# Kernel optimization log

Measured on AMD Instinct MI355X. Metric: run time of the kernel, lower is better.

## Reference

```python
import jax, jax.numpy as jnp
import numpy as np

N_NODES = 50000
N_EDGES = 800000
D_IN = 128
D_OUT = 128


def setup_inputs() -> dict:
    key = jax.random.key(0)
    k1, k2, k3, k4 = jax.random.split(key, 4)
    feature = jax.random.normal(k1, (N_NODES, D_IN), dtype=jnp.float32)
    edge_src = jax.random.randint(k2, (N_EDGES,), 0, N_NODES, dtype=jnp.int32)
    edge_dst = jax.random.randint(k3, (N_EDGES,), 0, N_NODES, dtype=jnp.int32)
    W = jax.random.normal(k4, (D_IN, D_OUT), dtype=jnp.float32) * (1.0 / np.sqrt(D_IN))
    b = jnp.zeros((D_OUT,), dtype=jnp.float32)
    return {"feature": feature, "edge_src": edge_src, "edge_dst": edge_dst, "W": W, "b": b}


def reference(feature, edge_src, edge_dst, W, b):
    # copy_src + sum reduce: for each edge, copy src node feature, sum into dst node
    msgs = feature[edge_src]  # [E, D_IN] gather
    h = jax.ops.segment_sum(msgs, edge_dst, num_segments=N_NODES)  # [N, D_IN]
    # linear + activation (relu)
    return jax.nn.relu(h @ W + b)
```

## Files before the change

kernel.cpp:

```cpp
#include <hip/hip_runtime.h>
#include <hip/hip_fp16.h>


constexpr int N    = 50000;
constexpr int E    = 800000;
constexpr int D    = 128;
constexpr int CAP  = 64;
constexpr int NT   = 3125;
constexpr int ZSTR = 136;
constexpr int NR   = 196;
constexpr int HB   = 256;
constexpr int EPB  = E / HB;

using f16x8 = __attribute__((ext_vector_type(8))) _Float16;
using f32x4 = __attribute__((ext_vector_type(4))) float;

__global__ void setup(const float* __restrict__ W, _Float16* __restrict__ Wf) {
    int t = blockIdx.x * 256 + threadIdx.x;
    int ct = t >> 8, ks = (t >> 6) & 3, lane = t & 63;
    int q = lane >> 4, li = lane & 15;
    _Float16 v[8];
    #pragma unroll
    for (int j = 0; j < 8; ++j)
        v[j] = (_Float16)W[(ks * 32 + q * 8 + j) * D + ct * 16 + li];
    *(f16x8*)(Wf + (size_t)t * 8) = *(const f16x8*)v;
}

__global__ __launch_bounds__(256) void midk(
        const float* __restrict__ feature,
        const int*   __restrict__ edst,
        const _Float16* __restrict__ Wf,
        int* __restrict__ hist,
        _Float16* __restrict__ Z) {
    __shared__ int h[NR];
    __shared__ _Float16 zs[4][16 * ZSTR];
    const int tid = threadIdx.x;

    if (blockIdx.x < HB) {
        const int b = blockIdx.x;
        if (tid < NR) h[tid] = 0;
        __syncthreads();
        const int e0 = b * EPB;
        for (int i = tid; i < EPB; i += 256)
            atomicAdd(&h[edst[e0 + i] >> 8], 1);
        __syncthreads();
        if (tid < NR) hist[b * NR + tid] = h[tid];
        return;
    }

    const int wave = tid >> 6, lane = tid & 63;
    const int wt = (blockIdx.x - HB) * 4 + wave;
    if (wt >= NT) return;
    const int q = lane >> 4, li = lane & 15;

    const float* fp = feature + (size_t)(wt * 16 + li) * D + q * 8;
    f16x8 afr[4];
    #pragma unroll
    for (int ks = 0; ks < 4; ++ks) {
        const float4 u0 = *(const float4*)(fp + ks * 32);
        const float4 u1 = *(const float4*)(fp + ks * 32 + 4);
        afr[ks][0] = (_Float16)u0.x; afr[ks][1] = (_Float16)u0.y;
        afr[ks][2] = (_Float16)u0.z; afr[ks][3] = (_Float16)u0.w;
        afr[ks][4] = (_Float16)u1.x; afr[ks][5] = (_Float16)u1.y;
        afr[ks][6] = (_Float16)u1.z; afr[ks][7] = (_Float16)u1.w;
    }

    f32x4 acc[8];
    #pragma unroll
    for (int ct = 0; ct < 8; ++ct) acc[ct] = (f32x4){0.f, 0.f, 0.f, 0.f};
    #pragma unroll
    for (int ks = 0; ks < 4; ++ks)
        #pragma unroll
        for (int ct = 0; ct < 8; ++ct) {
            const f16x8 b = *(const f16x8*)(Wf + (size_t)((ct * 4 + ks) * 64 + lane) * 8);
            acc[ct] = __builtin_amdgcn_mfma_f32_16x16x32_f16(afr[ks], b, acc[ct], 0, 0, 0);
        }

    _Float16* zt = zs[wave];
    #pragma unroll
    for (int ct = 0; ct < 8; ++ct)
        #pragma unroll
        for (int r = 0; r < 4; ++r)
            zt[(q * 4 + r) * ZSTR + ct * 16 + li] = (_Float16)acc[ct][r];
    #pragma unroll
    for (int it = 0; it < 4; ++it) {
        const f16x8 v = *(const f16x8*)(zt + (it * 4 + q) * ZSTR + li * 8);
        *(f16x8*)(Z + (size_t)(wt * 16 + it * 4 + q) * D + li * 8) = v;
    }
}

__global__ void scank(int* __restrict__ hist, int* __restrict__ total) {
    const int r    = blockIdx.x;
    const int lane = threadIdx.x;
    int h[4], sum = 0;
    #pragma unroll
    for (int j = 0; j < 4; ++j) {
        h[j] = hist[(lane * 4 + j) * NR + r];
        sum += h[j];
    }
    int incl = sum;
    #pragma unroll
    for (int off = 1; off < 64; off <<= 1) {
        int u = __shfl_up(incl, off);
        if (lane >= off) incl += u;
    }
    int run = incl - sum;
    #pragma unroll
    for (int j = 0; j < 4; ++j) {
        hist[(lane * 4 + j) * NR + r] = run;
        run += h[j];
    }
    if (lane == 63) total[r] = run;
}

__global__ __launch_bounds__(256) void partk(
        const int* __restrict__ esrc,
        const int* __restrict__ edst,
        const int* __restrict__ blockBase,
        const int* __restrict__ total,
        int* __restrict__ rangeStartG,
        unsigned int* __restrict__ part) {
    __shared__ int rs[NR];
    __shared__ int mb[NR];
    __shared__ int rk[NR];
    const int tid = threadIdx.x;
    const int b   = blockIdx.x;

    if (tid < 64) {
        int carry = 0;
        #pragma unroll
        for (int c = 0; c < 4; ++c) {
            int idx = c * 64 + tid;
            int v = (idx < NR) ? total[idx] : 0;
            int incl = v;
            #pragma unroll
            for (int off = 1; off < 64; off <<= 1) {
                int u = __shfl_up(incl, off);
                if (tid >= off) incl += u;
            }
            if (idx < NR) rs[idx] = incl - v + carry;
            carry += __shfl(incl, 63);
        }
    }
    if (tid < NR) { mb[tid] = blockBase[b * NR + tid]; rk[tid] = 0; }
    __syncthreads();
    if (b == 0 && tid < NR) rangeStartG[tid] = rs[tid];

    const int e0 = b * EPB;
    for (int i = tid; i < EPB; i += 256) {
        const int s = esrc[e0 + i];
        const int d = edst[e0 + i];
        const int r = d >> 8;
        const int k = atomicAdd(&rk[r], 1);
        part[rs[r] + mb[r] + k] = ((unsigned)(d & 255) << 16) | (unsigned)s;
    }
}

__global__ __launch_bounds__(256) void csrk(
        const unsigned int* __restrict__ part,
        const int* __restrict__ rangeStart,
        const int* __restrict__ total,
        unsigned short* __restrict__ bucket,
        int* __restrict__ cnt) {
    __shared__ int deg[256];
    const int r = blockIdx.x, tid = threadIdx.x;
    deg[tid] = 0;
    __syncthreads();
    const int rs = rangeStart[r], tot = total[r];
    for (int i = tid; i < tot; i += 256) {
        const unsigned p = part[rs + i];
        const int local = p >> 16;
        const int src   = p & 0xFFFF;
        const int k = atomicAdd(&deg[local], 1);
        if (k < CAP)
            bucket[(((size_t)r << 8) + local) * CAP + k] = (unsigned short)src;
    }
    __syncthreads();
    const int node = (r << 8) + tid;
    if (node < N) cnt[node] = deg[tid];
}

__global__ __launch_bounds__(256) void gather(
        const _Float16* __restrict__ Z,
        const int* __restrict__ cnt,
        const unsigned short* __restrict__ bucket,
        const float* __restrict__ bias,
        float* __restrict__ out) {
    const int tid  = threadIdx.x;
    const int wave = tid >> 6, lane = tid & 63;
    const int g    = lane >> 4, li = lane & 15;
    const int nA   = blockIdx.x * 8 + wave * 2;
    const int nB   = nA + 1;

    const int degA = min(cnt[nA], CAP);
    const int degB = min(cnt[nB], CAP);
    const int srcA = bucket[nA * CAP + lane];
    const int srcB = bucket[nB * CAP + lane];
    const float4 b0 = *(const float4*)(bias + li * 8);
    const float4 b1 = *(const float4*)(bias + li * 8 + 4);

    float accA[8] = {0,0,0,0,0,0,0,0};
    float accB[8] = {0,0,0,0,0,0,0,0};

    const int mx = max(degA, degB);
    for (int base = 0; base < mx; base += 16) {
        f16x8 hA[4], hB[4];
        float mA[4], mB[4];
        #pragma unroll
        for (int t = 0; t < 4; ++t) {
            const int r  = base + t * 4 + g;
            const int sA = __shfl(srcA, min(r, max(degA - 1, 0)));
            const int sB = __shfl(srcB, min(r, max(degB - 1, 0)));
            mA[t] = (r < degA) ? 1.f : 0.f;
            mB[t] = (r < degB) ? 1.f : 0.f;
            hA[t] = *(const f16x8*)(Z + (size_t)sA * D + li * 8);
            hB[t] = *(const f16x8*)(Z + (size_t)sB * D + li * 8);
        }
        #pragma unroll
        for (int t = 0; t < 4; ++t)
            #pragma unroll
            for (int j = 0; j < 8; ++j) {
                accA[j] += mA[t] * (float)hA[t][j];
                accB[j] += mB[t] * (float)hB[t][j];
            }
    }

    #pragma unroll
    for (int j = 0; j < 8; ++j) {
        accA[j] += __shfl_xor(accA[j], 16);
        accA[j] += __shfl_xor(accA[j], 32);
        accB[j] += __shfl_xor(accB[j], 16);
        accB[j] += __shfl_xor(accB[j], 32);
    }

    if (g == 0) {
        float4 o0, o1;
        o0.x = fmaxf(accA[0] + b0.x, 0.f); o0.y = fmaxf(accA[1] + b0.y, 0.f);
        o0.z = fmaxf(accA[2] + b0.z, 0.f); o0.w = fmaxf(accA[3] + b0.w, 0.f);
        o1.x = fmaxf(accA[4] + b1.x, 0.f); o1.y = fmaxf(accA[5] + b1.y, 0.f);
        o1.z = fmaxf(accA[6] + b1.z, 0.f); o1.w = fmaxf(accA[7] + b1.w, 0.f);
        float* op = out + (size_t)nA * D + li * 8;
        *(float4*)op       = o0;
        *(float4*)(op + 4) = o1;
    } else if (g == 1) {
        float4 o0, o1;
        o0.x = fmaxf(accB[0] + b0.x, 0.f); o0.y = fmaxf(accB[1] + b0.y, 0.f);
        o0.z = fmaxf(accB[2] + b0.z, 0.f); o0.w = fmaxf(accB[3] + b0.w, 0.f);
        o1.x = fmaxf(accB[4] + b1.x, 0.f); o1.y = fmaxf(accB[5] + b1.y, 0.f);
        o1.z = fmaxf(accB[6] + b1.z, 0.f); o1.w = fmaxf(accB[7] + b1.w, 0.f);
        float* op = out + (size_t)nB * D + li * 8;
        *(float4*)op       = o0;
        *(float4*)(op + 4) = o1;
    }
}

extern "C" void kernel_launch(void* const* d_in, const int* in_sizes, int n_in,
                              void* d_out, int out_size, void* d_ws, size_t ws_size,
                              hipStream_t stream) {
    const float* feature = (const float*)d_in[0];
    const int*   esrc    = (const int*)d_in[1];
    const int*   edst    = (const int*)d_in[2];
    const float* W       = (const float*)d_in[3];
    const float* bias    = (const float*)d_in[4];
    float*       out     = (float*)d_out;

    int*            cnt    = (int*)d_ws;
    unsigned short* bucket = (unsigned short*)(cnt + N);
    _Float16*       Z      = (_Float16*)(bucket + (size_t)N * CAP);
    _Float16*       Wf     = Z + (size_t)N * D;
    int*            hist   = (int*)(Wf + 16384);
    int*            total  = hist + HB * NR;
    int*            rangeS = total + NR;
    unsigned int*   part   = (unsigned int*)(rangeS + NR);

    setup<<<8, 256, 0, stream>>>(W, Wf);
    midk <<<HB + (NT + 3) / 4, 256, 0, stream>>>(feature, edst, Wf, hist, Z);
    scank<<<NR, 64, 0, stream>>>(hist, total);
    partk<<<HB, 256, 0, stream>>>(esrc, edst, hist, total, rangeS, part);
    csrk <<<NR, 256, 0, stream>>>(part, rangeS, total, bucket, cnt);
    gather<<<N / 8, 256, 0, stream>>>(Z, cnt, bucket, bias, out);
}
```

Measured before the change: 152.0 us.

## Fuse CSR bucketing into gather kernel using shared-memory buckets per 64-node range

Merges the CSR bucket-build kernel and the gather kernel into one. Each block now handles a 64-node destination range and builds its neighbour lists in shared memory instead of global memory, which removes the global bucket and count arrays and one kernel launch. Invalid neighbour slots are redirected to a zero row appended to Z, which replaces the per-edge mask multiply. The histogram, scan and partition kernels are rescaled to 782 ranges and 500 histogram blocks. Trade-off: only 782 blocks run the gather, each with four waves looping over eight node pairs, so there is less parallelism and latency hiding than the previous 6250-block gather.

```diff
diff --git a/kernel.cpp b/kernel.cpp
--- a/kernel.cpp
+++ b/kernel.cpp
@@ -8,14 +8,19 @@
 constexpr int CAP  = 64;
 constexpr int NT   = 3125;
 constexpr int ZSTR = 136;
-constexpr int NR   = 196;
-constexpr int HB   = 256;
+constexpr int NR   = 782;
+constexpr int HB   = 500;
 constexpr int EPB  = E / HB;
 
 using f16x8 = __attribute__((ext_vector_type(8))) _Float16;
 using f32x4 = __attribute__((ext_vector_type(4))) float;
 
-__global__ void setup(const float* __restrict__ W, _Float16* __restrict__ Wf) {
+__global__ void setup(const float* __restrict__ W, _Float16* __restrict__ Wf,
+                      _Float16* __restrict__ Z) {
+    if (blockIdx.x == 8) {
+        if (threadIdx.x < D) Z[(size_t)N * D + threadIdx.x] = (_Float16)0.f;
+        return;
+    }
     int t = blockIdx.x * 256 + threadIdx.x;
     int ct = t >> 8, ks = (t >> 6) & 3, lane = t & 63;
     int q = lane >> 4, li = lane & 15;
@@ -38,13 +43,13 @@
 
     if (blockIdx.x < HB) {
         const int b = blockIdx.x;
-        if (tid < NR) h[tid] = 0;
+        for (int i = tid; i < NR; i += 256) h[i] = 0;
         __syncthreads();
         const int e0 = b * EPB;
         for (int i = tid; i < EPB; i += 256)
-            atomicAdd(&h[edst[e0 + i] >> 8], 1);
+            atomicAdd(&h[edst[e0 + i] >> 6], 1);
         __syncthreads();
-        if (tid < NR) hist[b * NR + tid] = h[tid];
+        for (int i = tid; i < NR; i += 256) hist[b * NR + i] = h[i];
         return;
     }
 
@@ -92,10 +97,11 @@
 __global__ void scank(int* __restrict__ hist, int* __restrict__ total) {
     const int r    = blockIdx.x;
     const int lane = threadIdx.x;
-    int h[4], sum = 0;
-    #pragma unroll
-    for (int j = 0; j < 4; ++j) {
-        h[j] = hist[(lane * 4 + j) * NR + r];
+    int h[8], sum = 0;
+    #pragma unroll
+    for (int j = 0; j < 8; ++j) {
+        const int idx = lane * 8 + j;
+        h[j] = (idx < HB) ? hist[idx * NR + r] : 0;
         sum += h[j];
     }
     int incl = sum;
@@ -106,8 +112,9 @@
     }
     int run = incl - sum;
     #pragma unroll
-    for (int j = 0; j < 4; ++j) {
-        hist[(lane * 4 + j) * NR + r] = run;
+    for (int j = 0; j < 8; ++j) {
+        const int idx = lane * 8 + j;
+        if (idx < HB) hist[idx * NR + r] = run;
         run += h[j];
     }
     if (lane == 63) total[r] = run;
@@ -129,9 +136,9 @@
     if (tid < 64) {
         int carry = 0;
         #pragma unroll
-        for (int c = 0; c < 4; ++c) {
-            int idx = c * 64 + tid;
-            int v = (idx < NR) ? total[idx] : 0;
+        for (int c = 0; c < 13; ++c) {
+            const int idx = c * 64 + tid;
+            const int v = (idx < NR) ? total[idx] : 0;
             int incl = v;
             #pragma unroll
             for (int off = 1; off < 64; off <<= 1) {
@@ -142,115 +149,109 @@
             carry += __shfl(incl, 63);
         }
     }
-    if (tid < NR) { mb[tid] = blockBase[b * NR + tid]; rk[tid] = 0; }
+    for (int i = tid; i < NR; i += 256) { mb[i] = blockBase[b * NR + i]; rk[i] = 0; }
     __syncthreads();
-    if (b == 0 && tid < NR) rangeStartG[tid] = rs[tid];
+    if (b == 0)
+        for (int i = tid; i < NR; i += 256) rangeStartG[i] = rs[i];
 
     const int e0 = b * EPB;
     for (int i = tid; i < EPB; i += 256) {
         const int s = esrc[e0 + i];
         const int d = edst[e0 + i];
-        const int r = d >> 8;
+        const int r = d >> 6;
         const int k = atomicAdd(&rk[r], 1);
-        part[rs[r] + mb[r] + k] = ((unsigned)(d & 255) << 16) | (unsigned)s;
-    }
-}
-
-__global__ __launch_bounds__(256) void csrk(
+        part[rs[r] + mb[r] + k] = ((unsigned)(d & 63) << 16) | (unsigned)s;
+    }
+}
+
+__global__ __launch_bounds__(256) void csrgather(
         const unsigned int* __restrict__ part,
         const int* __restrict__ rangeStart,
         const int* __restrict__ total,
-        unsigned short* __restrict__ bucket,
-        int* __restrict__ cnt) {
-    __shared__ int deg[256];
+        const _Float16* __restrict__ Z,
+        const float* __restrict__ bias,
+        float* __restrict__ out) {
+    __shared__ unsigned short bkt[64 * CAP];
+    __shared__ int deg[64];
     const int r = blockIdx.x, tid = threadIdx.x;
-    deg[tid] = 0;
+
+    if (tid < 64) deg[tid] = 0;
     __syncthreads();
-    const int rs = rangeStart[r], tot = total[r];
+    const int rsv = rangeStart[r], tot = total[r];
     for (int i = tid; i < tot; i += 256) {
-        const unsigned p = part[rs + i];
+        const unsigned p = part[rsv + i];
         const int local = p >> 16;
         const int src   = p & 0xFFFF;
         const int k = atomicAdd(&deg[local], 1);
-        if (k < CAP)
-            bucket[(((size_t)r << 8) + local) * CAP + k] = (unsigned short)src;
+        if (k < CAP) bkt[local * CAP + k] = (unsigned short)src;
     }
     __syncthreads();
-    const int node = (r << 8) + tid;
-    if (node < N) cnt[node] = deg[tid];
-}
-
-__global__ __launch_bounds__(256) void gather(
-        const _Float16* __restrict__ Z,
-        const int* __restrict__ cnt,
-        const unsigned short* __restrict__ bucket,
-        const float* __restrict__ bias,
-        float* __restrict__ out) {
-    const int tid  = threadIdx.x;
+
     const int wave = tid >> 6, lane = tid & 63;
-    const int g    = lane >> 4, li = lane & 15;
-    const int nA   = blockIdx.x * 8 + wave * 2;
-    const int nB   = nA + 1;
-
-    const int degA = min(cnt[nA], CAP);
-    const int degB = min(cnt[nB], CAP);
-    const int srcA = bucket[nA * CAP + lane];
-    const int srcB = bucket[nB * CAP + lane];
+    const int g = lane >> 4, li = lane & 15;
     const float4 b0 = *(const float4*)(bias + li * 8);
     const float4 b1 = *(const float4*)(bias + li * 8 + 4);
 
-    float accA[8] = {0,0,0,0,0,0,0,0};
-    float accB[8] = {0,0,0,0,0,0,0,0};
-
-    const int mx = max(degA, degB);
-    for (int base = 0; base < mx; base += 16) {
-        f16x8 hA[4], hB[4];
-        float mA[4], mB[4];
-        #pragma unroll
-        for (int t = 0; t < 4; ++t) {
-            const int r  = base + t * 4 + g;
-            const int sA = __shfl(srcA, min(r, max(degA - 1, 0)));
-            const int sB = __shfl(srcB, min(r, max(degB - 1, 0)));
-            mA[t] = (r < degA) ? 1.f : 0.f;
-            mB[t] = (r < degB) ? 1.f : 0.f;
-            hA[t] = *(const f16x8*)(Z + (size_t)sA * D + li * 8);
-            hB[t] = *(const f16x8*)(Z + (size_t)sB * D + li * 8);
-        }
-        #pragma unroll
-        for (int t = 0; t < 4; ++t)
+    for (int pair = 0; pair < 8; ++pair) {
+        const int lA = wave * 16 + pair * 2;
+        const int lB = lA + 1;
+        const int degA = min(deg[lA], CAP);
+        const int degB = min(deg[lB], CAP);
+
+        float accA[8] = {0,0,0,0,0,0,0,0};
+        float accB[8] = {0,0,0,0,0,0,0,0};
+
+        const int mx = max(degA, degB);
+        for (int base = 0; base < mx; base += 16) {
+            f16x8 hA[4], hB[4];
             #pragma unroll
-            for (int j = 0; j < 8; ++j) {
-                accA[j] += mA[t] * (float)hA[t][j];
-                accB[j] += mB[t] * (float)hB[t][j];
+            for (int t = 0; t < 4; ++t) {
+                const int rr = base + t * 4 + g;
+                int sA = bkt[lA * CAP + rr];
+                int sB = bkt[lB * CAP + rr];
+                sA = (rr < degA) ? sA : N;
+                sB = (rr < degB) ? sB : N;
+                hA[t] = *(const f16x8*)(Z + (size_t)sA * D + li * 8);
+                hB[t] = *(const f16x8*)(Z + (size_t)sB * D + li * 8);
             }
-    }
-
-    #pragma unroll
-    for (int j = 0; j < 8; ++j) {
-        accA[j] += __shfl_xor(accA[j], 16);
-        accA[j] += __shfl_xor(accA[j], 32);
-        accB[j] += __shfl_xor(accB[j], 16);
-        accB[j] += __shfl_xor(accB[j], 32);
-    }
-
-    if (g == 0) {
-        float4 o0, o1;
-        o0.x = fmaxf(accA[0] + b0.x, 0.f); o0.y = fmaxf(accA[1] + b0.y, 0.f);
-        o0.z = fmaxf(accA[2] + b0.z, 0.f); o0.w = fmaxf(accA[3] + b0.w, 0.f);
-        o1.x = fmaxf(accA[4] + b1.x, 0.f); o1.y = fmaxf(accA[5] + b1.y, 0.f);
-        o1.z = fmaxf(accA[6] + b1.z, 0.f); o1.w = fmaxf(accA[7] + b1.w, 0.f);
-        float* op = out + (size_t)nA * D + li * 8;
-        *(float4*)op       = o0;
-        *(float4*)(op + 4) = o1;
-    } else if (g == 1) {
-        float4 o0, o1;
-        o0.x = fmaxf(accB[0] + b0.x, 0.f); o0.y = fmaxf(accB[1] + b0.y, 0.f);
-        o0.z = fmaxf(accB[2] + b0.z, 0.f); o0.w = fmaxf(accB[3] + b0.w, 0.f);
-        o1.x = fmaxf(accB[4] + b1.x, 0.f); o1.y = fmaxf(accB[5] + b1.y, 0.f);
-        o1.z = fmaxf(accB[6] + b1.z, 0.f); o1.w = fmaxf(accB[7] + b1.w, 0.f);
-        float* op = out + (size_t)nB * D + li * 8;
-        *(float4*)op       = o0;
-        *(float4*)(op + 4) = o1;
+            #pragma unroll
+            for (int t = 0; t < 4; ++t)
+                #pragma unroll
+                for (int j = 0; j < 8; ++j) {
+                    accA[j] += (float)hA[t][j];
+                    accB[j] += (float)hB[t][j];
+                }
+        }
+
+        #pragma unroll
+        for (int j = 0; j < 8; ++j) {
+            accA[j] += __shfl_xor(accA[j], 16);
+            accA[j] += __shfl_xor(accA[j], 32);
+            accB[j] += __shfl_xor(accB[j], 16);
+            accB[j] += __shfl_xor(accB[j], 32);
+        }
+
+        const int nodeA = (r << 6) + lA;
+        const int nodeB = (r << 6) + lB;
+        if (g == 0 && nodeA < N) {
+            float4 o0, o1;
+            o0.x = fmaxf(accA[0] + b0.x, 0.f); o0.y = fmaxf(accA[1] + b0.y, 0.f);
+            o0.z = fmaxf(accA[2] + b0.z, 0.f); o0.w = fmaxf(accA[3] + b0.w, 0.f);
+            o1.x = fmaxf(accA[4] + b1.x, 0.f); o1.y = fmaxf(accA[5] + b1.y, 0.f);
+            o1.z = fmaxf(accA[6] + b1.z, 0.f); o1.w = fmaxf(accA[7] + b1.w, 0.f);
+            float* op = out + (size_t)nodeA * D + li * 8;
+            *(float4*)op       = o0;
+            *(float4*)(op + 4) = o1;
+        } else if (g == 1 && nodeB < N) {
+            float4 o0, o1;
+            o0.x = fmaxf(accB[0] + b0.x, 0.f); o0.y = fmaxf(accB[1] + b0.y, 0.f);
+            o0.z = fmaxf(accB[2] + b0.z, 0.f); o0.w = fmaxf(accB[3] + b0.w, 0.f);
+            o1.x = fmaxf(accB[4] + b1.x, 0.f); o1.y = fmaxf(accB[5] + b1.y, 0.f);
+            o1.z = fmaxf(accB[6] + b1.z, 0.f); o1.w = fmaxf(accB[7] + b1.w, 0.f);
+            float* op = out + (size_t)nodeB * D + li * 8;
+            *(float4*)op       = o0;
+            *(float4*)(op + 4) = o1;
+        }
     }
 }
 
@@ -264,19 +265,16 @@
     const float* bias    = (const float*)d_in[4];
     float*       out     = (float*)d_out;
 
-    int*            cnt    = (int*)d_ws;
-    unsigned short* bucket = (unsigned short*)(cnt + N);
-    _Float16*       Z      = (_Float16*)(bucket + (size_t)N * CAP);
-    _Float16*       Wf     = Z + (size_t)N * D;
-    int*            hist   = (int*)(Wf + 16384);
-    int*            total  = hist + HB * NR;
-    int*            rangeS = total + NR;
-    unsigned int*   part   = (unsigned int*)(rangeS + NR);
-
-    setup<<<8, 256, 0, stream>>>(W, Wf);
+    _Float16*     Z      = (_Float16*)d_ws;
+    _Float16*     Wf     = Z + (size_t)(N + 1) * D;
+    int*          hist   = (int*)(Wf + 16384);
+    int*          total  = hist + HB * NR;
+    int*          rangeS = total + NR;
+    unsigned int* part   = (unsigned int*)(rangeS + NR);
+
+    setup<<<9, 256, 0, stream>>>(W, Wf, Z);
     midk <<<HB + (NT + 3) / 4, 256, 0, stream>>>(feature, edst, Wf, hist, Z);
     scank<<<NR, 64, 0, stream>>>(hist, total);
     partk<<<HB, 256, 0, stream>>>(esrc, edst, hist, total, rangeS, part);
-    csrk <<<NR, 256, 0, stream>>>(part, rangeS, total, bucket, cnt);
-    gather<<<N / 8, 256, 0, stream>>>(Z, cnt, bucket, bias, out);
-}
+    csrgather<<<NR, 256, 0, stream>>>(part, rangeS, total, Z, bias, out);
+}
```

Result: faster. 145.1 us (-4.5%).
